# Performance work log

Measured on AMD Instinct MI355X. Metric: run time of the kernel, lower is better.

## Reference

```python
import math
import jax, jax.numpy as jnp
import numpy as np

INPUT_DIM = 1024
OUTPUT_DIM = 1024
DEGREE = 8
EPS = 1.0


def setup_inputs() -> dict:
    key = jax.random.key(0)
    k1, k2 = jax.random.split(key)
    x = jax.random.normal(k1, (8192, INPUT_DIM), dtype=jnp.float32)
    std = 1.0 / (INPUT_DIM * (DEGREE + 1))
    hermite_coeffs = std * jax.random.normal(k2, (INPUT_DIM, OUTPUT_DIM, DEGREE + 1), dtype=jnp.float32)
    return {"x": x, "hermite_coeffs": hermite_coeffs}


def _hermite_basis(x):
    # x: [B, I] squashed input; returns [B, I, DEGREE+1] Hermite-function basis.
    pi_q = math.pi ** (-0.25)
    gauss = jnp.exp(-0.5 * x * x)
    h0 = pi_q * gauss
    hs = [h0]
    if DEGREE > 0:
        hs.append(math.sqrt(2.0) * pi_q * x * gauss)
    for i in range(2, DEGREE + 1):
        hs.append(math.sqrt(2.0 / i) * x * hs[i - 1] - math.sqrt((i - 1) / i) * hs[i - 2])
    return jnp.stack(hs, axis=-1)


def reference(x, hermite_coeffs):
    x = x.reshape(-1, INPUT_DIM)
    x = jnp.tanh(x) * (math.sqrt(2 * DEGREE + 1) + EPS)
    hermite = _hermite_basis(x)  # [B, I, D+1]
    y = jnp.einsum('bid,iod->bo', hermite, hermite_coeffs)
    return y.reshape(-1, OUTPUT_DIM)
```

## Files before the change

### kernel.cpp

```cpp
#include <hip/hip_runtime.h>

#define MDIM 8192
#define IDIM 1024
#define ODIM 1024
#define D1   9
#define KDIM (IDIM * D1)
#define KHALF (KDIM / 2)

typedef _Float16 half8   __attribute__((ext_vector_type(8)));
typedef float    float4v __attribute__((ext_vector_type(4)));

#define BSCALE 256.0f
#define INV_BSCALE (1.0f / 256.0f)
#define USCALE 5.123105625617661f
#define H0C 0.7511255444649425f
#define SQRT2 1.4142135623730951f

__constant__ float c1a[D1] = {0.f, 0.f, 1.0f, 0.8164965809277260f, 0.7071067811865476f,
                              0.6324555320336759f, 0.5773502691896258f, 0.5345224838248488f, 0.5f};
__constant__ float c2a[D1] = {0.f, 0.f, 0.7071067811865476f, 0.8164965809277260f, 0.8660254037844386f,
                              0.8944271909999159f, 0.9128709291752769f, 0.9258200997725514f, 0.9354143466934853f};

__device__ __forceinline__ void hermite9(float xv, float h[D1]) {
    float ax = fabsf(xv);
    float t  = __expf(-2.0f * ax);
    float th = (1.0f - t) * __builtin_amdgcn_rcpf(1.0f + t);
    th = copysignf(th, xv);
    float u = th * USCALE;
    float g = __expf(-0.5f * u * u);
    h[0] = H0C * g;
    h[1] = SQRT2 * H0C * u * g;
#pragma unroll
    for (int d = 2; d < D1; ++d) h[d] = c1a[d] * u * h[d - 1] - c2a[d] * h[d - 2];
}

__global__ __launch_bounds__(256) void prep_all(const float* __restrict__ C,
                                                _Float16* __restrict__ Bt,
                                                const float* __restrict__ x,
                                                _Float16* __restrict__ H) {
    if (blockIdx.x < 1024) {
        __shared__ float lds[288 * 33];
        const int t  = threadIdx.x;
        const int ti = blockIdx.x & 31;
        const int to = blockIdx.x >> 5;
        const float* base = C + (size_t)ti * 32 * 9216 + (size_t)to * 32 * 9;
#pragma unroll
        for (int j = 0; j < 36; ++j) {
            int f   = t + 256 * j;
            int row = f / 288;
            int col = f - row * 288;
            lds[col * 33 + row] = base[(size_t)row * 9216 + col];
        }
        __syncthreads();
        _Float16* bb = Bt + (size_t)to * 32 * KDIM + ti * 32;
#pragma unroll
        for (int j = 0; j < 36; ++j) {
            int e   = t + 256 * j;
            int i   = e & 31;
            int odp = e >> 5;
            int ol  = odp / 9;
            int d   = odp - ol * 9;
            bb[(size_t)ol * KDIM + d * IDIM + i] = (_Float16)(lds[odp * 33 + i] * BSCALE);
        }
    } else {
        int t  = (blockIdx.x - 1024) * 256 + threadIdx.x;
        int r  = t >> 7;
        int ig = (t & 127) << 3;
        const float* xp = x + (((size_t)r) << 10) + ig;
        float4 a0 = *(const float4*)xp;
        float4 a1 = *(const float4*)(xp + 4);
        float xv[8] = {a0.x, a0.y, a0.z, a0.w, a1.x, a1.y, a1.z, a1.w};
        float h[8][D1];
#pragma unroll
        for (int e = 0; e < 8; ++e) hermite9(xv[e], h[e]);
        _Float16* hp = H + (size_t)r * KDIM + ig;
#pragma unroll
        for (int d = 0; d < D1; ++d) {
            half8 v;
#pragma unroll
            for (int e = 0; e < 8; ++e) v[e] = (_Float16)h[e][d];
            *(half8*)(hp + (size_t)d * IDIM) = v;
        }
    }
}

__global__ __launch_bounds__(256, 4) void gemm_hf(
    const _Float16* __restrict__ A,
    const _Float16* __restrict__ Bt,
    float* __restrict__ out)
{
    const int tid = threadIdx.x;
    const int w = tid >> 6;
    const int l = tid & 63;
    const int bn = blockIdx.x;
    const int bm = blockIdx.y;
    const int kb0 = blockIdx.z * KHALF;

    __shared__ _Float16 As[128 * 64];
    __shared__ _Float16 Bs[128 * 64];

    const int lrow8 = l >> 3;
    const int kgrp  = (l & 7) ^ lrow8;
    const _Float16* Ag = A  + ((size_t)(bm * 128 + w * 8 + lrow8) * KDIM + kb0 + kgrp * 8);
    const _Float16* Bg = Bt + ((size_t)(bn * 128 + w * 8 + lrow8) * KDIM + kb0 + kgrp * 8);

    const int q   = l >> 4;
    const int m16 = l & 15;
    const int s3  = m16 & 7;
    const int wm  = w >> 1, wn = w & 1;

    float4v acc[4][4] = {};

    for (int k0 = 0; k0 < KHALF; k0 += 64) {
#pragma unroll
        for (int r = 0; r < 4; ++r) {
            __builtin_amdgcn_global_load_lds(
                (const __attribute__((address_space(1))) void*)(Ag + (size_t)(r * 32) * KDIM + k0),
                (__attribute__((address_space(3))) void*)((char*)As + (r * 4 + w) * 1024),
                16, 0, 0);
            __builtin_amdgcn_global_load_lds(
                (const __attribute__((address_space(1))) void*)(Bg + (size_t)(r * 32) * KDIM + k0),
                (__attribute__((address_space(3))) void*)((char*)Bs + (r * 4 + w) * 1024),
                16, 0, 0);
        }
        __syncthreads();

#pragma unroll
        for (int ko = 0; ko < 2; ++ko) {
            const int slot = (q + 4 * ko) ^ s3;
            half8 af[4], bf[4];
#pragma unroll
            for (int i = 0; i < 4; ++i) {
                af[i] = *(const half8*)&As[(wm * 64 + i * 16 + m16) * 64 + slot * 8];
                bf[i] = *(const half8*)&Bs[(wn * 64 + i * 16 + m16) * 64 + slot * 8];
            }
#pragma unroll
            for (int i = 0; i < 4; ++i)
#pragma unroll
                for (int j = 0; j < 4; ++j)
                    acc[i][j] = __builtin_amdgcn_mfma_f32_16x16x32_f16(af[i], bf[j], acc[i][j], 0, 0, 0);
        }
        __syncthreads();
    }

#pragma unroll
    for (int i = 0; i < 4; ++i) {
        int row = bm * 128 + wm * 64 + i * 16 + q * 4;
#pragma unroll
        for (int j = 0; j < 4; ++j) {
            int col = bn * 128 + wn * 64 + j * 16 + m16;
            float* op = out + (size_t)row * ODIM + col;
#pragma unroll
            for (int r2 = 0; r2 < 4; ++r2)
                atomicAdd(op + (size_t)r2 * ODIM, acc[i][j][r2] * INV_BSCALE);
        }
    }
}

__global__ void naive_kernel(const float* __restrict__ x, const float* __restrict__ C,
                             float* __restrict__ out) {
    __shared__ float hb[IDIM * D1];
    int b = blockIdx.x;
    int tid = threadIdx.x;
    for (int i = tid; i < IDIM; i += 256) {
        float h[D1];
        hermite9(x[(size_t)b * IDIM + i], h);
#pragma unroll
        for (int d = 0; d < D1; ++d) hb[i * D1 + d] = h[d];
    }
    __syncthreads();
    for (int o = tid; o < ODIM; o += 256) {
        float acc = 0.f;
        for (int i = 0; i < IDIM; ++i) {
            const float* cp = C + ((size_t)i * ODIM + o) * D1;
            const float* hp = hb + i * D1;
#pragma unroll
            for (int d = 0; d < D1; ++d) acc += hp[d] * cp[d];
        }
        out[(size_t)b * ODIM + o] = acc;
    }
}

extern "C" void kernel_launch(void* const* d_in, const int* in_sizes, int n_in,
                              void* d_out, int out_size, void* d_ws, size_t ws_size,
                              hipStream_t stream) {
    const float* x      = (const float*)d_in[0];
    const float* coeffs = (const float*)d_in[1];
    float* out = (float*)d_out;

    const size_t bt_bytes = (size_t)ODIM * KDIM * sizeof(_Float16);
    const size_t h_bytes  = (size_t)MDIM * KDIM * sizeof(_Float16);

    if (ws_size >= bt_bytes + h_bytes) {
        _Float16* Bt = (_Float16*)d_ws;
        _Float16* H  = (_Float16*)((char*)d_ws + bt_bytes);
        hipMemsetAsync(out, 0, (size_t)out_size * sizeof(float), stream);
        hipLaunchKernelGGL(prep_all, dim3(1024 + (MDIM * IDIM) / 2048), dim3(256), 0, stream,
                           coeffs, Bt, x, H);
        hipLaunchKernelGGL(gemm_hf, dim3(8, 64, 2), dim3(256), 0, stream, H, Bt, out);
    } else {
        hipLaunchKernelGGL(naive_kernel, dim3(MDIM), dim3(256), 0, stream, x, coeffs, out);
    }
}
```

Measured before the change: 331.4 us.

## Double-buffer GEMM LDS tiles and drop split-K atomics and memset

The GEMM now double-buffers its A/B shared-memory tiles so global-to-LDS loads for the next K step overlap MFMA compute on the current one. It removes the two-way split-K, so each block covers the full K range and writes results with plain stores instead of atomics, and the output memset is dropped. The cost is doubled LDS use and an occupancy hint lowered from 4 to 2, and the grid halves to 512 blocks, which reduces parallelism across the CUs.

```diff
diff --git a/kernel.cpp b/kernel.cpp
--- a/kernel.cpp
+++ b/kernel.cpp
@@ -5,7 +5,7 @@
 #define ODIM 1024
 #define D1   9
 #define KDIM (IDIM * D1)
-#define KHALF (KDIM / 2)
+#define NSTEP (KDIM / 64)
 
 typedef _Float16 half8   __attribute__((ext_vector_type(8)));
 typedef float    float4v __attribute__((ext_vector_type(4)));
@@ -84,7 +84,7 @@
     }
 }
 
-__global__ __launch_bounds__(256, 4) void gemm_hf(
+__global__ __launch_bounds__(256, 2) void gemm_db(
     const _Float16* __restrict__ A,
     const _Float16* __restrict__ Bt,
     float* __restrict__ out)
@@ -94,15 +94,14 @@
     const int l = tid & 63;
     const int bn = blockIdx.x;
     const int bm = blockIdx.y;
-    const int kb0 = blockIdx.z * KHALF;
-
-    __shared__ _Float16 As[128 * 64];
-    __shared__ _Float16 Bs[128 * 64];
+
+    __shared__ _Float16 As[2][128 * 64];
+    __shared__ _Float16 Bs[2][128 * 64];
 
     const int lrow8 = l >> 3;
     const int kgrp  = (l & 7) ^ lrow8;
-    const _Float16* Ag = A  + ((size_t)(bm * 128 + w * 8 + lrow8) * KDIM + kb0 + kgrp * 8);
-    const _Float16* Bg = Bt + ((size_t)(bn * 128 + w * 8 + lrow8) * KDIM + kb0 + kgrp * 8);
+    const _Float16* Ag = A  + ((size_t)(bm * 128 + w * 8 + lrow8) * KDIM + kgrp * 8);
+    const _Float16* Bg = Bt + ((size_t)(bn * 128 + w * 8 + lrow8) * KDIM + kgrp * 8);
 
     const int q   = l >> 4;
     const int m16 = l & 15;
@@ -111,28 +110,29 @@
 
     float4v acc[4][4] = {};
 
-    for (int k0 = 0; k0 < KHALF; k0 += 64) {
+    auto stage = [&](int buf, int k0) {
 #pragma unroll
         for (int r = 0; r < 4; ++r) {
             __builtin_amdgcn_global_load_lds(
                 (const __attribute__((address_space(1))) void*)(Ag + (size_t)(r * 32) * KDIM + k0),
-                (__attribute__((address_space(3))) void*)((char*)As + (r * 4 + w) * 1024),
+                (__attribute__((address_space(3))) void*)((char*)&As[buf][0] + (r * 4 + w) * 1024),
                 16, 0, 0);
             __builtin_amdgcn_global_load_lds(
                 (const __attribute__((address_space(1))) void*)(Bg + (size_t)(r * 32) * KDIM + k0),
-                (__attribute__((address_space(3))) void*)((char*)Bs + (r * 4 + w) * 1024),
+                (__attribute__((address_space(3))) void*)((char*)&Bs[buf][0] + (r * 4 + w) * 1024),
                 16, 0, 0);
         }
-        __syncthreads();
-
+    };
+
+    auto compute = [&](int buf) {
 #pragma unroll
         for (int ko = 0; ko < 2; ++ko) {
             const int slot = (q + 4 * ko) ^ s3;
             half8 af[4], bf[4];
 #pragma unroll
             for (int i = 0; i < 4; ++i) {
-                af[i] = *(const half8*)&As[(wm * 64 + i * 16 + m16) * 64 + slot * 8];
-                bf[i] = *(const half8*)&Bs[(wn * 64 + i * 16 + m16) * 64 + slot * 8];
+                af[i] = *(const half8*)&As[buf][(wm * 64 + i * 16 + m16) * 64 + slot * 8];
+                bf[i] = *(const half8*)&Bs[buf][(wn * 64 + i * 16 + m16) * 64 + slot * 8];
             }
 #pragma unroll
             for (int i = 0; i < 4; ++i)
@@ -140,7 +140,17 @@
                 for (int j = 0; j < 4; ++j)
                     acc[i][j] = __builtin_amdgcn_mfma_f32_16x16x32_f16(af[i], bf[j], acc[i][j], 0, 0, 0);
         }
+    };
+
+    stage(0, 0);
+
+    for (int s2 = 0; s2 < NSTEP; s2 += 2) {
         __syncthreads();
+        stage(1, (s2 + 1) * 64);
+        compute(0);
+        __syncthreads();
+        if (s2 + 2 < NSTEP) stage(0, (s2 + 2) * 64);
+        compute(1);
     }
 
 #pragma unroll
@@ -152,7 +162,7 @@
             float* op = out + (size_t)row * ODIM + col;
 #pragma unroll
             for (int r2 = 0; r2 < 4; ++r2)
-                atomicAdd(op + (size_t)r2 * ODIM, acc[i][j][r2] * INV_BSCALE);
+                op[(size_t)r2 * ODIM] = acc[i][j][r2] * INV_BSCALE;
         }
     }
 }
@@ -194,10 +204,9 @@
     if (ws_size >= bt_bytes + h_bytes) {
         _Float16* Bt = (_Float16*)d_ws;
         _Float16* H  = (_Float16*)((char*)d_ws + bt_bytes);
-        hipMemsetAsync(out, 0, (size_t)out_size * sizeof(float), stream);
         hipLaunchKernelGGL(prep_all, dim3(1024 + (MDIM * IDIM) / 2048), dim3(256), 0, stream,
                            coeffs, Bt, x, H);
-        hipLaunchKernelGGL(gemm_hf, dim3(8, 64, 2), dim3(256), 0, stream, H, Bt, out);
+        hipLaunchKernelGGL(gemm_db, dim3(8, 64), dim3(256), 0, stream, H, Bt, out);
     } else {
         hipLaunchKernelGGL(naive_kernel, dim3(MDIM), dim3(256), 0, stream, x, coeffs, out);
     }
```

After: 303.6 us. 8.4% less time.
